# Kernel optimization log

Measured on AMD Instinct MI355X. Metric: run time of the kernel, lower is better.

The kernel has to match this reference:

```python
import jax, jax.numpy as jnp
import numpy as np

LN_EPS = 1e-5
TOP_K = 2

def _layer_norm(x, g, b):
    m = jnp.mean(x, axis=-1, keepdims=True)
    v = jnp.var(x, axis=-1, keepdims=True)
    return (x - m) * jax.lax.rsqrt(v + LN_EPS) * g + b

def _skew(X, pad_value):
    # shift every row one step right: [B,M,L] -> [B,M,M+L]
    B, M, L = X.shape
    X = jnp.pad(X, ((0, 0), (0, 0), (0, M + 1)), constant_values=pad_value)
    X = X.reshape(B, -1)[:, :-M]
    return X.reshape(B, M, M + L)

def _unskew(X):
    # reverse of _skew: [B,M,M+L] -> [B,M,L]
    B, M, Lt = X.shape
    L = Lt - M
    X = X.reshape(B, -1)
    X = jnp.pad(X, ((0, 0), (0, M)))
    return X.reshape(B, M, M + L + 1)[:, :, :L]

def _heads(x, K, D):
    # [B,T,H] -> [B*K,T,D]
    B, T, _ = x.shape
    return x.reshape(B, T, K, D).transpose(0, 2, 1, 3).reshape(B * K, T, D)

def setup_inputs() -> dict:
    key = jax.random.key(0)
    ks = jax.random.split(key, 12)
    B, M, L, H, Dh, E, Kh = 4, 512, 512, 1024, 2048, 8, 8
    D = H // Kh
    s = 0.02
    return {
        "h": jax.random.normal(ks[0], (B, M, H), jnp.float32),
        "h_cache": jax.random.normal(ks[1], (B, L, H), jnp.float32),
        "key_pe": jax.random.normal(ks[2], (1, D, L), jnp.float32) * s,
        "Wq": jax.random.normal(ks[3], (H, H), jnp.float32) * s,
        "Wk": jax.random.normal(ks[4], (H, H), jnp.float32) * s,
        "Wv": jax.random.normal(ks[5], (H, H), jnp.float32) * s,
        "Wo": jax.random.normal(ks[6], (H, H), jnp.float32) * s,
        "ln1_g": jnp.ones((H,), jnp.float32),
        "ln1_b": jnp.zeros((H,), jnp.float32),
        "gate_W": jax.random.normal(ks[7], (H, E), jnp.float32) * s,
        "gate_b": jnp.zeros((E,), jnp.float32),
        "W1": jax.random.normal(ks[8], (E, H, Dh), jnp.float32) * s,
        "b1": jnp.zeros((E, Dh), jnp.float32),
        "W2": jax.random.normal(ks[9], (E, Dh, H), jnp.float32) * s,
        "b2": jnp.zeros((E, H), jnp.float32),
        "ln2_g": jnp.ones((H,), jnp.float32),
        "ln2_b": jnp.zeros((H,), jnp.float32),
    }

def reference(h, h_cache, key_pe, Wq, Wk, Wv, Wo, ln1_g, ln1_b,
              gate_W, gate_b, W1, b1, W2, b2, ln2_g, ln2_b):
    B, M, H = h.shape
    L = h_cache.shape[1]
    Kh = 8
    D = H // Kh
    # --- multi-head relative-position attention over (cache, current) ---
    h_all = jnp.concatenate([h_cache, h], axis=1)            # [B, L+M, H]
    q = _heads(h @ Wq, Kh, D)                                # [B*K, M, D]
    k = _heads(h_all @ Wk, Kh, D)                            # [B*K, M+L, D]
    v = _heads(h_all @ Wv, Kh, D)                            # [B*K, M+L, D]
    attn_cont = _unskew(jnp.einsum('bmd,bnd->bmn', q, k))    # [B*K, M, L]
    attn_pos = jnp.einsum('bmd,xdl->bml', q, key_pe)         # [B*K, M, L]
    attn = jax.nn.softmax((attn_cont + attn_pos) / jnp.sqrt(jnp.float32(D)), axis=-1)
    out = jnp.einsum('bmn,bnd->bmd', _skew(attn, 0.0), v)    # [B*K, M, D]
    out = out.reshape(B, Kh, M, D).transpose(0, 2, 1, 3).reshape(B, M, H)
    attn_out = out @ Wo
    h1 = _layer_norm(h + attn_out, ln1_g, ln1_b)             # post-LN residual
    # --- top-k gated MoE FFN (NaiveGate), post-LN residual ---
    x = h1.reshape(-1, H)                                    # [N, H]
    N = x.shape[0]
    E = gate_b.shape[0]
    logits = x @ gate_W + gate_b                             # [N, E]
    top_val, top_idx = jax.lax.top_k(logits, TOP_K)          # [N, k]
    scores = jax.nn.softmax(top_val, axis=-1)                # [N, k]
    combine = jnp.zeros((N, E), x.dtype).at[jnp.arange(N)[:, None], top_idx].add(scores)
    he = jax.nn.relu(jnp.einsum('nh,ehf->enf', x, W1) + b1[:, None, :])  # [E, N, Dh]
    ye = jnp.einsum('enf,efh->enh', he, W2) + b2[:, None, :]             # [E, N, H]
    core = jnp.einsum('ne,enh->nh', combine, ye).reshape(B, M, H)
    output = _layer_norm(h1 + core, ln2_g, ln2_b)
    return output, top_idx
```

## Files before the change

kernel.cpp:

```cpp
#include <hip/hip_runtime.h>
#include <hip/hip_bf16.h>
#include <stdint.h>


typedef _Float16 f16;
typedef _Float16 f16x8 __attribute__((ext_vector_type(8)));
typedef _Float16 f16x4 __attribute__((ext_vector_type(4)));
typedef float    f32x4 __attribute__((ext_vector_type(4)));
typedef int      i32x4 __attribute__((ext_vector_type(4)));

#define MFMA16(a, b, c) __builtin_amdgcn_mfma_f32_16x16x32_f16((a), (b), (c), 0, 0, 0)
#define LO_SCALE 2048.0f
#define LO_INV   4.8828125e-4f

__device__ __forceinline__ void split2(float x, f16* h, f16* l) {
  f16 hh = (f16)x;
  *h = hh;
  *l = (f16)((x - (float)hh) * LO_SCALE);
}

__device__ __forceinline__ f32x4 zero4() {
  f32x4 z; z[0] = 0.f; z[1] = 0.f; z[2] = 0.f; z[3] = 0.f; return z;
}

__global__ void __launch_bounds__(256) cast_hall_k(const float* __restrict__ h,
                                                   const float* __restrict__ hc,
                                                   f16* __restrict__ hi,
                                                   f16* __restrict__ lo) {
  int c = blockIdx.x * 256 + threadIdx.x;
  int e0 = c * 8;
  int row = e0 >> 10;
  int col = e0 & 1023;
  int b = row >> 10, pos = row & 1023;
  const float* src = (pos < 512) ? (hc + (size_t)((b << 9) + pos) * 1024 + col)
                                 : (h  + (size_t)((b << 9) + (pos - 512)) * 1024 + col);
  float4 v0 = ((const float4*)src)[0];
  float4 v1 = ((const float4*)src)[1];
  float xs[8] = {v0.x, v0.y, v0.z, v0.w, v1.x, v1.y, v1.z, v1.w};
  f16x8 vh, vl;
#pragma unroll
  for (int i = 0; i < 8; i++) { f16 a, bb; split2(xs[i], &a, &bb); vh[i] = a; vl[i] = bb; }
  *(f16x8*)&hi[e0] = vh;
  *(f16x8*)&lo[e0] = vl;
}

template <int SPLIT>
__global__ void __launch_bounds__(256) transpose_cast_k(const float* __restrict__ in,
                                                        f16* __restrict__ oh,
                                                        f16* __restrict__ ol,
                                                        int R, int C) {
  in += (size_t)blockIdx.z * R * C;
  oh += (size_t)blockIdx.z * R * C;
  if constexpr (SPLIT) ol += (size_t)blockIdx.z * R * C;
  __shared__ float tile[32][33];
  int c0 = blockIdx.x * 32, r0 = blockIdx.y * 32;
  int tr = threadIdx.x >> 3, tc = (threadIdx.x & 7) * 4;
  float4 v = *(const float4*)&in[(size_t)(r0 + tr) * C + c0 + tc];
  tile[tr][tc + 0] = v.x; tile[tr][tc + 1] = v.y; tile[tr][tc + 2] = v.z; tile[tr][tc + 3] = v.w;
  __syncthreads();
  int oc = tr;
  int orr = tc;
  f16x4 vh, vl;
#pragma unroll
  for (int i = 0; i < 4; i++) {
    float x = tile[orr + i][oc];
    f16 a, bb; split2(x, &a, &bb);
    vh[i] = a; vl[i] = bb;
  }
  *(f16x4*)&oh[(size_t)(c0 + oc) * R + r0 + orr] = vh;
  if constexpr (SPLIT) *(f16x4*)&ol[(size_t)(c0 + oc) * R + r0 + orr] = vl;
}

#define AM_ID 0
#define AM_Q  1
#define AM_GA 2
#define AM_PA 3
#define EP_QK 0
#define EP_VT 1
#define EP_F32 2
#define EP_HE 3
#define EP_YE 4

template <int SPLIT, int AMAP, int EPI>
__global__ void __launch_bounds__(256) gemm_k(
    const f16* __restrict__ Ah, const f16* __restrict__ Al,
    const f16* __restrict__ Bh, const f16* __restrict__ Bl,
    void* __restrict__ o0, void* __restrict__ o1,
    const float* __restrict__ bias,
    int Kd, int strideA, int lgRPB, int bExpStride,
    const int* __restrict__ list, const int* __restrict__ bases,
    const int* __restrict__ counts) {
  constexpr int PL = SPLIT ? 2 : 1;
  constexpr int BN = SPLIT ? 64 : 128;
  constexpr int NT = BN / 32;
  const int e = blockIdx.z;
  int cnt = 0, base0 = 0;
  if constexpr (AMAP == AM_GA || AMAP == AM_PA) {
    cnt = counts[e]; base0 = bases[e];
    if ((int)blockIdx.y * 128 >= cnt) return;
    Bh += (size_t)e * bExpStride;
  }
  __shared__ f16 sA[PL][128 * 32];
  __shared__ f16 sB[PL][BN * 32];
  const int n0 = blockIdx.x * BN, r0 = blockIdx.y * 128;
  const int tid = threadIdx.x, lane = tid & 63, wv = tid >> 6;
  const int wm = (wv >> 1) * 64, wn = (wv & 1) * (BN / 2);

  f32x4 accM[4][NT], accC[4][NT];
#pragma unroll
  for (int i = 0; i < 4; i++)
#pragma unroll
    for (int j = 0; j < NT; j++) { accM[i][j] = zero4(); accC[i][j] = zero4(); }

  int aRow[2], aCu[2];
#pragma unroll
  for (int c = 0; c < 2; c++) {
    int u = c * 256 + tid;
    int r = u >> 2, cu = u & 3;
    aCu[c] = ((cu ^ ((r >> 1) & 3)) << 3);
    int rr = r0 + r;
    int g;
    if constexpr (AMAP == AM_ID) g = rr;
    else if constexpr (AMAP == AM_Q) g = ((rr >> 9) << 10) + 512 + (rr & 511);
    else if constexpr (AMAP == AM_GA) g = (rr < cnt) ? list[base0 + rr] : 0;
    else g = base0 + rr;
    aRow[c] = g;
  }

  for (int k0 = 0; k0 < Kd; k0 += 32) {
#pragma unroll
    for (int c = 0; c < 2; c++) {
      int u = c * 256 + tid;
      int scol = k0 + aCu[c];
      *(f16x8*)&sA[0][u * 8] = *(const f16x8*)&Ah[(size_t)aRow[c] * strideA + scol];
      if constexpr (SPLIT)
        *(f16x8*)&sA[1][u * 8] = *(const f16x8*)&Al[(size_t)aRow[c] * strideA + scol];
    }
#pragma unroll
    for (int c = 0; c * 256 < BN * 4; c++) {
      int u = c * 256 + tid;
      int r = u >> 2, cu = u & 3;
      int scol = k0 + ((cu ^ ((r >> 1) & 3)) << 3);
      int gb = n0 + r;
      *(f16x8*)&sB[0][u * 8] = *(const f16x8*)&Bh[(size_t)gb * Kd + scol];
      if constexpr (SPLIT)
        *(f16x8*)&sB[1][u * 8] = *(const f16x8*)&Bl[(size_t)gb * Kd + scol];
    }
    __syncthreads();

    f16x8 ah[4], al[4];
#pragma unroll
    for (int mt = 0; mt < 4; mt++) {
      int r = wm + mt * 16 + (lane & 15);
      int cu = (lane >> 4) ^ ((r >> 1) & 3);
      ah[mt] = *(const f16x8*)&sA[0][(r * 4 + cu) * 8];
      if constexpr (SPLIT) al[mt] = *(const f16x8*)&sA[1][(r * 4 + cu) * 8];
    }
#pragma unroll
    for (int nt = 0; nt < NT; nt++) {
      int r = wn + nt * 16 + (lane & 15);
      int cu = (lane >> 4) ^ ((r >> 1) & 3);
      f16x8 bh = *(const f16x8*)&sB[0][(r * 4 + cu) * 8];
      f16x8 bl;
      if constexpr (SPLIT) bl = *(const f16x8*)&sB[1][(r * 4 + cu) * 8];
#pragma unroll
      for (int mt = 0; mt < 4; mt++) {
        accM[mt][nt] = MFMA16(ah[mt], bh, accM[mt][nt]);
        if constexpr (SPLIT) {
          accC[mt][nt] = MFMA16(ah[mt], bl, accC[mt][nt]);
          accC[mt][nt] = MFMA16(al[mt], bh, accC[mt][nt]);
        }
      }
    }
    __syncthreads();
  }

#pragma unroll
  for (int mt = 0; mt < 4; mt++)
#pragma unroll
    for (int nt = 0; nt < NT; nt++)
#pragma unroll
      for (int rg = 0; rg < 4; rg++) {
        int row = r0 + wm + mt * 16 + ((lane >> 4) << 2) + rg;
        int col = n0 + wn + nt * 16 + (lane & 15);
        float v = accM[mt][nt][rg];
        if constexpr (SPLIT) v += accC[mt][nt][rg] * LO_INV;
        if constexpr (EPI == EP_QK) {
          int bq = row >> lgRPB, pos = row & ((1 << lgRPB) - 1);
          size_t ad = ((size_t)((((bq << 3) + (col >> 7)) << lgRPB) + pos)) * 128 + (col & 127);
          f16 hh, ll; split2(v, &hh, &ll);
          ((f16*)o0)[ad] = hh; ((f16*)o1)[ad] = ll;
        } else if constexpr (EPI == EP_VT) {
          size_t ad = ((size_t)(((row >> 10) << 3) + (col >> 7)) * 128 + (col & 127)) * 1024 + (row & 1023);
          f16 hh, ll; split2(v, &hh, &ll);
          ((f16*)o0)[ad] = hh; ((f16*)o1)[ad] = ll;
        } else if constexpr (EPI == EP_F32) {
          ((float*)o0)[(size_t)row * 1024 + col] = v;
        } else if constexpr (EPI == EP_HE) {
          if (row < cnt) {
            float t = v + bias[(e << 11) + col];
            ((f16*)o0)[(size_t)(base0 + row) * 2048 + col] = (f16)fmaxf(t, 0.f);
          }
        } else if constexpr (EPI == EP_YE) {
          if (row < cnt)
            ((float*)o0)[(size_t)(base0 + row) * 1024 + col] = v + bias[(e << 10) + col];
        }
      }
}

__device__ __forceinline__ void unpack_p(const unsigned* sp, f16x8* hi, f16x8* lo) {
  i32x4 u0 = *(const i32x4*)sp;
  i32x4 u1 = *(const i32x4*)(sp + 4);
  i32x4 h, l;
  h[0] = (u0[0] & 0xffff) | (u0[1] << 16);
  h[1] = (u0[2] & 0xffff) | (u0[3] << 16);
  h[2] = (u1[0] & 0xffff) | (u1[1] << 16);
  h[3] = (u1[2] & 0xffff) | (u1[3] << 16);
  l[0] = (int)(((unsigned)u0[0] >> 16) | ((unsigned)u0[1] & 0xffff0000u));
  l[1] = (int)(((unsigned)u0[2] >> 16) | ((unsigned)u0[3] & 0xffff0000u));
  l[2] = (int)(((unsigned)u1[0] >> 16) | ((unsigned)u1[1] & 0xffff0000u));
  l[3] = (int)(((unsigned)u1[2] >> 16) | ((unsigned)u1[3] & 0xffff0000u));
  *hi = __builtin_bit_cast(f16x8, h);
  *lo = __builtin_bit_cast(f16x8, l);
}

__global__ void __launch_bounds__(256) attn_k(
    const f16* __restrict__ qh_, const f16* __restrict__ ql_,
    const f16* __restrict__ kh_, const f16* __restrict__ kl_,
    const f16* __restrict__ ph_, const f16* __restrict__ pl_,
    const f16* __restrict__ vh_, const f16* __restrict__ vl_,
    f16* __restrict__ oh_, f16* __restrict__ ol_) {
  __shared__ float S[32][548];
  const int bh = blockIdx.y;
  const int m0 = blockIdx.x * 32;
  const int tid = threadIdx.x, lane = tid & 63, wv = tid >> 6;
  const int lr = lane & 15, lgp = lane >> 4;

  f16x8 qh[2][4], ql[2][4];
  {
    const size_t qbase = ((size_t)bh * 512 + m0) * 128;
#pragma unroll
    for (int mt = 0; mt < 2; mt++)
#pragma unroll
      for (int kb = 0; kb < 4; kb++) {
        size_t off = qbase + (size_t)(mt * 16 + lr) * 128 + kb * 32 + lgp * 8;
        qh[mt][kb] = *(const f16x8*)&qh_[off];
        ql[mt][kb] = *(const f16x8*)&ql_[off];
      }
  }

  {
    const size_t kbase = ((size_t)bh * 1024 + m0) * 128;
    int ntB = (wv < 2) ? wv * 9 : 18 + (wv - 2) * 8;
    int ntE = ntB + ((wv < 2) ? 9 : 8);
    for (int nt = ntB; nt < ntE; ++nt) {
      f16x8 kh[4], kl[4];
#pragma unroll
      for (int kb = 0; kb < 4; kb++) {
        size_t off = kbase + (size_t)(nt * 16 + lr) * 128 + kb * 32 + lgp * 8;
        kh[kb] = *(const f16x8*)&kh_[off];
        kl[kb] = *(const f16x8*)&kl_[off];
      }
      f32x4 aM[2], aC[2];
      aM[0] = zero4(); aM[1] = zero4(); aC[0] = zero4(); aC[1] = zero4();
#pragma unroll
      for (int kb = 0; kb < 4; kb++)
#pragma unroll
        for (int mt = 0; mt < 2; mt++) {
          aM[mt] = MFMA16(qh[mt][kb], kh[kb], aM[mt]);
          aC[mt] = MFMA16(qh[mt][kb], kl[kb], aC[mt]);
          aC[mt] = MFMA16(ql[mt][kb], kh[kb], aC[mt]);
        }
#pragma unroll
      for (int mt = 0; mt < 2; mt++)
#pragma unroll
        for (int rg = 0; rg < 4; rg++) {
          int m = mt * 16 + lgp * 4 + rg;
          S[m][nt * 16 + lr] = aM[mt][rg] + aC[mt][rg] * LO_INV;
        }
    }
  }
  __syncthreads();

  {
    for (int lt = wv * 8; lt < wv * 8 + 8; ++lt) {
      f16x8 eh[4], el[4];
#pragma unroll
      for (int kb = 0; kb < 4; kb++) {
        size_t off = (size_t)(lt * 16 + lr) * 128 + kb * 32 + lgp * 8;
        eh[kb] = *(const f16x8*)&ph_[off];
        el[kb] = *(const f16x8*)&pl_[off];
      }
      f32x4 aM[2], aC[2];
      aM[0] = zero4(); aM[1] = zero4(); aC[0] = zero4(); aC[1] = zero4();
#pragma unroll
      for (int kb = 0; kb < 4; kb++)
#pragma unroll
        for (int mt = 0; mt < 2; mt++) {
          aM[mt] = MFMA16(qh[mt][kb], eh[kb], aM[mt]);
          aC[mt] = MFMA16(qh[mt][kb], el[kb], aC[mt]);
          aC[mt] = MFMA16(ql[mt][kb], eh[kb], aC[mt]);
        }
#pragma unroll
      for (int mt = 0; mt < 2; mt++)
#pragma unroll
        for (int rg = 0; rg < 4; rg++) {
          int m = mt * 16 + lgp * 4 + rg;
          int lc = lt * 16 + lr;
          S[m][m + lc] += aM[mt][rg] + aC[mt][rg] * LO_INV;
        }
    }
  }
  __syncthreads();

  {
    const float scl = 0.08838834764831843f;
    for (int rr = 0; rr < 8; ++rr) {
      int m = wv * 8 + rr;
      float mx = -3.0e38f;
#pragma unroll
      for (int it = 0; it < 9; ++it) {
        int j = it * 64 + lane;
        if (j < 544 && j >= m && j < m + 512) mx = fmaxf(mx, S[m][j]);
      }
#pragma unroll
      for (int o = 32; o > 0; o >>= 1) mx = fmaxf(mx, __shfl_xor(mx, o));
      float pv[9]; float sm = 0.f;
#pragma unroll
      for (int it = 0; it < 9; ++it) {
        int j = it * 64 + lane;
        float p = 0.f;
        if (j < 544 && j >= m && j < m + 512) p = expf((S[m][j] - mx) * scl);
        pv[it] = p; sm += p;
      }
#pragma unroll
      for (int o = 32; o > 0; o >>= 1) sm += __shfl_xor(sm, o);
      float inv = 1.0f / sm;
#pragma unroll
      for (int it = 0; it < 9; ++it) {
        int j = it * 64 + lane;
        if (j < 544) {
          float pn = pv[it] * inv;
          f16 hh, ll; split2(pn, &hh, &ll);
          unsigned pk = (unsigned)__builtin_bit_cast(unsigned short, hh) |
                        ((unsigned)__builtin_bit_cast(unsigned short, ll) << 16);
          ((unsigned*)&S[m][0])[j] = pk;
        }
      }
    }
  }
  __syncthreads();

  f32x4 accM[2][2], accC[2][2];
#pragma unroll
  for (int i = 0; i < 2; i++)
#pragma unroll
    for (int j = 0; j < 2; j++) { accM[i][j] = zero4(); accC[i][j] = zero4(); }
  for (int kb = 0; kb < 17; ++kb) {
    f16x8 pah[2], pal[2];
#pragma unroll
    for (int mt = 0; mt < 2; mt++) {
      const unsigned* sp = (const unsigned*)&S[mt * 16 + lr][0] + kb * 32 + lgp * 8;
      unpack_p(sp, &pah[mt], &pal[mt]);
    }
#pragma unroll
    for (int ntl = 0; ntl < 2; ++ntl) {
      int d = wv * 32 + ntl * 16 + lr;
      size_t off = ((size_t)bh * 128 + d) * 1024 + m0 + kb * 32 + lgp * 8;
      f16x8 vh = *(const f16x8*)&vh_[off];
      f16x8 vl = *(const f16x8*)&vl_[off];
#pragma unroll
      for (int mt = 0; mt < 2; mt++) {
        accM[mt][ntl] = MFMA16(pah[mt], vh, accM[mt][ntl]);
        accC[mt][ntl] = MFMA16(pah[mt], vl, accC[mt][ntl]);
        accC[mt][ntl] = MFMA16(pal[mt], vh, accC[mt][ntl]);
      }
    }
  }
  const int b = bh >> 3, hd = bh & 7;
#pragma unroll
  for (int mt = 0; mt < 2; mt++)
#pragma unroll
    for (int ntl = 0; ntl < 2; ntl++)
#pragma unroll
      for (int rg = 0; rg < 4; rg++) {
        int m = mt * 16 + lgp * 4 + rg;
        int d = wv * 32 + ntl * 16 + lr;
        float v = accM[mt][ntl][rg] + accC[mt][ntl][rg] * LO_INV;
        size_t ad = ((size_t)(b * 512 + m0 + m)) * 1024 + hd * 128 + d;
        f16 hh, ll; split2(v, &hh, &ll);
        oh_[ad] = hh; ol_[ad] = ll;
      }
}

__device__ __forceinline__ float blk_sum(float v, float* red) {
#pragma unroll
  for (int o = 32; o > 0; o >>= 1) v += __shfl_xor(v, o);
  int wv = threadIdx.x >> 6;
  if ((threadIdx.x & 63) == 0) red[wv] = v;
  __syncthreads();
  float r = red[0] + red[1] + red[2] + red[3];
  __syncthreads();
  return r;
}

__global__ void __launch_bounds__(256) ln1_k(const float* __restrict__ h,
                                             const float* __restrict__ ap,
                                             const float* __restrict__ g,
                                             const float* __restrict__ bb,
                                             float* __restrict__ h1,
                                             f16* __restrict__ h1h) {
  int row = blockIdx.x;
  __shared__ float red[4];
  float4 hv = ((const float4*)(h + (size_t)row * 1024))[threadIdx.x];
  float4 av = ((const float4*)(ap + (size_t)row * 1024))[threadIdx.x];
  float4 x; x.x = hv.x + av.x; x.y = hv.y + av.y; x.z = hv.z + av.z; x.w = hv.w + av.w;
  float s = x.x + x.y + x.z + x.w;
  s = blk_sum(s, red);
  float mean = s * (1.0f / 1024.0f);
  float4 d; d.x = x.x - mean; d.y = x.y - mean; d.z = x.z - mean; d.w = x.w - mean;
  float s2 = d.x * d.x + d.y * d.y + d.z * d.z + d.w * d.w;
  s2 = blk_sum(s2, red);
  float var = s2 * (1.0f / 1024.0f);
  float inv = 1.0f / sqrtf(var + 1e-5f);
  float4 gv = ((const float4*)g)[threadIdx.x];
  float4 bv = ((const float4*)bb)[threadIdx.x];
  float4 y; y.x = d.x * inv * gv.x + bv.x; y.y = d.y * inv * gv.y + bv.y;
  y.z = d.z * inv * gv.z + bv.z; y.w = d.w * inv * gv.w + bv.w;
  ((float4*)(h1 + (size_t)row * 1024))[threadIdx.x] = y;
  f16x4 yh; yh[0] = (f16)y.x; yh[1] = (f16)y.y; yh[2] = (f16)y.z; yh[3] = (f16)y.w;
  *(f16x4*)&h1h[(size_t)row * 1024 + threadIdx.x * 4] = yh;
}

__global__ void __launch_bounds__(256) gate_k(const float* __restrict__ h1,
                                              const float* __restrict__ gW,
                                              const float* __restrict__ gb,
                                              float* __restrict__ outIdx,
                                              float* __restrict__ sc,
                                              int* __restrict__ te,
                                              int* __restrict__ ctrl) {
  int t = blockIdx.x * 4 + (threadIdx.x >> 6);
  int lane = threadIdx.x & 63;
  float a0 = 0, a1 = 0, a2 = 0, a3 = 0, a4 = 0, a5 = 0, a6 = 0, a7 = 0;
  for (int i = lane; i < 1024; i += 64) {
    float x = h1[(size_t)t * 1024 + i];
    const float4* w = (const float4*)&gW[i * 8];
    float4 w0 = w[0], w1 = w[1];
    a0 += x * w0.x; a1 += x * w0.y; a2 += x * w0.z; a3 += x * w0.w;
    a4 += x * w1.x; a5 += x * w1.y; a6 += x * w1.z; a7 += x * w1.w;
  }
  float av[8] = {a0, a1, a2, a3, a4, a5, a6, a7};
#pragma unroll
  for (int e = 0; e < 8; e++)
#pragma unroll
    for (int o = 32; o > 0; o >>= 1) av[e] += __shfl_xor(av[e], o);
  if (lane == 0) {
#pragma unroll
    for (int e = 0; e < 8; e++) av[e] += gb[e];
    int i0 = 0; float v0 = av[0];
#pragma unroll
    for (int e = 1; e < 8; e++) if (av[e] > v0) { v0 = av[e]; i0 = e; }
    int i1 = -1; float v1 = -3.0e38f;
#pragma unroll
    for (int e = 0; e < 8; e++) if (e != i0 && av[e] > v1) { v1 = av[e]; i1 = e; }
    float ex = expf(v1 - v0);
    float den = 1.0f + ex;
    outIdx[t * 2] = (float)i0; outIdx[t * 2 + 1] = (float)i1;
    sc[t * 2] = 1.0f / den; sc[t * 2 + 1] = ex / den;
    te[t * 2] = i0; te[t * 2 + 1] = i1;
    atomicAdd(&ctrl[i0], 1); atomicAdd(&ctrl[i1], 1);
  }
}

__global__ void scan_k(int* ctrl) {
  if (threadIdx.x == 0 && blockIdx.x == 0) {
    int s = 0;
    for (int e = 0; e < 8; e++) { ctrl[8 + e] = s; s += ctrl[e]; }
  }
}

__global__ void __launch_bounds__(256) scatter_k(const int* __restrict__ te,
                                                 int* ctrl,
                                                 int* __restrict__ list,
                                                 int* __restrict__ ppos) {
  int t = blockIdx.x * 256 + threadIdx.x;
  if (t >= 2048) return;
#pragma unroll
  for (int s = 0; s < 2; s++) {
    int e = te[t * 2 + s];
    int pos = atomicAdd(&ctrl[16 + e], 1);
    int pr = ctrl[8 + e] + pos;
    list[pr] = t;
    ppos[t * 2 + s] = pr;
  }
}

__global__ void __launch_bounds__(256) comb_ln2_k(const float* __restrict__ h1,
                                                  const float* __restrict__ ye,
                                                  const float* __restrict__ sc,
                                                  const int* __restrict__ ppos,
                                                  const float* __restrict__ g,
                                                  const float* __restrict__ bb,
                                                  float* __restrict__ out) {
  int row = blockIdx.x;
  __shared__ float red[4];
  int p0 = ppos[row * 2], p1 = ppos[row * 2 + 1];
  float s0 = sc[row * 2], s1 = sc[row * 2 + 1];
  float4 a = ((const float4*)(h1 + (size_t)row * 1024))[threadIdx.x];
  float4 y0 = ((const float4*)(ye + (size_t)p0 * 1024))[threadIdx.x];
  float4 y1 = ((const float4*)(ye + (size_t)p1 * 1024))[threadIdx.x];
  float4 x;
  x.x = a.x + s0 * y0.x + s1 * y1.x; x.y = a.y + s0 * y0.y + s1 * y1.y;
  x.z = a.z + s0 * y0.z + s1 * y1.z; x.w = a.w + s0 * y0.w + s1 * y1.w;
  float s = x.x + x.y + x.z + x.w;
  s = blk_sum(s, red);
  float mean = s * (1.0f / 1024.0f);
  float4 d; d.x = x.x - mean; d.y = x.y - mean; d.z = x.z - mean; d.w = x.w - mean;
  float s2 = d.x * d.x + d.y * d.y + d.z * d.z + d.w * d.w;
  s2 = blk_sum(s2, red);
  float var = s2 * (1.0f / 1024.0f);
  float inv = 1.0f / sqrtf(var + 1e-5f);
  float4 gv = ((const float4*)g)[threadIdx.x];
  float4 bv = ((const float4*)bb)[threadIdx.x];
  float4 y; y.x = d.x * inv * gv.x + bv.x; y.y = d.y * inv * gv.y + bv.y;
  y.z = d.z * inv * gv.z + bv.z; y.w = d.w * inv * gv.w + bv.w;
  ((float4*)(out + (size_t)row * 1024))[threadIdx.x] = y;
}

extern "C" void kernel_launch(void* const* d_in, const int* in_sizes, int n_in,
                              void* d_out, int out_size, void* d_ws, size_t ws_size,
                              hipStream_t stream) {
  const float* h   = (const float*)d_in[0];
  const float* hc  = (const float*)d_in[1];
  const float* pe  = (const float*)d_in[2];
  const float* Wq  = (const float*)d_in[3];
  const float* Wk  = (const float*)d_in[4];
  const float* Wv  = (const float*)d_in[5];
  const float* Wo  = (const float*)d_in[6];
  const float* g1  = (const float*)d_in[7];
  const float* b1n = (const float*)d_in[8];
  const float* gW  = (const float*)d_in[9];
  const float* gb  = (const float*)d_in[10];
  const float* W1  = (const float*)d_in[11];
  const float* b1e = (const float*)d_in[12];
  const float* W2  = (const float*)d_in[13];
  const float* b2e = (const float*)d_in[14];
  const float* g2  = (const float*)d_in[15];
  const float* b2n = (const float*)d_in[16];
  float* out = (float*)d_out;
  float* outIdx = out + 2097152;

  char* w = (char*)d_ws;
  size_t off = 0;
  auto alloc = [&](size_t bytes) -> char* {
    char* p = w + off;
    off += (bytes + 255) & ~(size_t)255;
    return p;
  };
  int*   ctrl  = (int*)alloc(128);
  f16*   hallH = (f16*)alloc(4096ull * 1024 * 2);
  f16*   hallL = (f16*)alloc(4096ull * 1024 * 2);
  f16*   WqtH  = (f16*)alloc(1024ull * 1024 * 2);
  f16*   WqtL  = (f16*)alloc(1024ull * 1024 * 2);
  f16*   WktH  = (f16*)alloc(1024ull * 1024 * 2);
  f16*   WktL  = (f16*)alloc(1024ull * 1024 * 2);
  f16*   WvtH  = (f16*)alloc(1024ull * 1024 * 2);
  f16*   WvtL  = (f16*)alloc(1024ull * 1024 * 2);
  f16*   WotH  = (f16*)alloc(1024ull * 1024 * 2);
  f16*   WotL  = (f16*)alloc(1024ull * 1024 * 2);
  f16*   peH   = (f16*)alloc(512ull * 128 * 2);
  f16*   peL   = (f16*)alloc(512ull * 128 * 2);
  f16*   qH    = (f16*)alloc(2097152ull * 2);
  f16*   qL    = (f16*)alloc(2097152ull * 2);
  f16*   kH    = (f16*)alloc(4194304ull * 2);
  f16*   kL    = (f16*)alloc(4194304ull * 2);
  f16*   vtH   = (f16*)alloc(4194304ull * 2);
  f16*   vtL   = (f16*)alloc(4194304ull * 2);
  f16*   attH  = (f16*)alloc(2097152ull * 2);
  f16*   attL  = (f16*)alloc(2097152ull * 2);
  float* aproj = (float*)alloc(2097152ull * 4);
  float* h1    = (float*)alloc(2097152ull * 4);
  f16*   h1h   = (f16*)alloc(2097152ull * 2);
  f16*   W1t   = (f16*)alloc(16777216ull * 2);
  f16*   W2t   = (f16*)alloc(16777216ull * 2);
  f16*   he    = (f16*)alloc(4224ull * 2048 * 2);
  float* ye    = (float*)alloc(4224ull * 1024 * 4);
  float* scb   = (float*)alloc(2048ull * 2 * 4);
  int*   te    = (int*)alloc(2048ull * 2 * 4);
  int*   ppos  = (int*)alloc(2048ull * 2 * 4);
  int*   list  = (int*)alloc(4096ull * 4);
  (void)in_sizes; (void)n_in; (void)out_size; (void)ws_size;

  hipMemsetAsync(ctrl, 0, 128, stream);

  cast_hall_k<<<2048, 256, 0, stream>>>(h, hc, hallH, hallL);
  transpose_cast_k<1><<<dim3(32, 32, 1), 256, 0, stream>>>(Wq, WqtH, WqtL, 1024, 1024);
  transpose_cast_k<1><<<dim3(32, 32, 1), 256, 0, stream>>>(Wk, WktH, WktL, 1024, 1024);
  transpose_cast_k<1><<<dim3(32, 32, 1), 256, 0, stream>>>(Wv, WvtH, WvtL, 1024, 1024);
  transpose_cast_k<1><<<dim3(32, 32, 1), 256, 0, stream>>>(Wo, WotH, WotL, 1024, 1024);
  transpose_cast_k<1><<<dim3(16, 4, 1), 256, 0, stream>>>(pe, peH, peL, 128, 512);
  transpose_cast_k<0><<<dim3(64, 32, 8), 256, 0, stream>>>(W1, W1t, nullptr, 1024, 2048);
  transpose_cast_k<0><<<dim3(32, 64, 8), 256, 0, stream>>>(W2, W2t, nullptr, 2048, 1024);

  gemm_k<1, AM_Q, EP_QK><<<dim3(16, 16, 1), 256, 0, stream>>>(
      hallH, hallL, WqtH, WqtL, qH, qL, nullptr, 1024, 1024, 9, 0, nullptr, nullptr, nullptr);
  gemm_k<1, AM_ID, EP_QK><<<dim3(16, 32, 1), 256, 0, stream>>>(
      hallH, hallL, WktH, WktL, kH, kL, nullptr, 1024, 1024, 10, 0, nullptr, nullptr, nullptr);
  gemm_k<1, AM_ID, EP_VT><<<dim3(16, 32, 1), 256, 0, stream>>>(
      hallH, hallL, WvtH, WvtL, vtH, vtL, nullptr, 1024, 1024, 10, 0, nullptr, nullptr, nullptr);

  attn_k<<<dim3(16, 32, 1), 256, 0, stream>>>(qH, qL, kH, kL, peH, peL, vtH, vtL, attH, attL);

  gemm_k<1, AM_ID, EP_F32><<<dim3(16, 16, 1), 256, 0, stream>>>(
      attH, attL, WotH, WotL, aproj, nullptr, nullptr, 1024, 1024, 0, 0, nullptr, nullptr, nullptr);
  ln1_k<<<2048, 256, 0, stream>>>(h, aproj, g1, b1n, h1, h1h);

  gate_k<<<512, 256, 0, stream>>>(h1, gW, gb, outIdx, scb, te, ctrl);
  scan_k<<<1, 64, 0, stream>>>(ctrl);
  scatter_k<<<8, 256, 0, stream>>>(te, ctrl, list, ppos);

  gemm_k<0, AM_GA, EP_HE><<<dim3(16, 16, 8), 256, 0, stream>>>(
      h1h, nullptr, W1t, nullptr, he, nullptr, b1e, 1024, 1024, 0, 2048 * 1024, list, ctrl + 8, ctrl);
  gemm_k<0, AM_PA, EP_YE><<<dim3(8, 16, 8), 256, 0, stream>>>(
      he, nullptr, W2t, nullptr, ye, nullptr, b2e, 2048, 2048, 0, 1024 * 2048, nullptr, ctrl + 8, ctrl);

  comb_ln2_k<<<2048, 256, 0, stream>>>(h1, ye, scb, ppos, g2, b2n, out);
}
```

Baseline: 646.0 us.

## Fuse Q/K/V projections into one GEMM and retile the other GEMMs

Concatenates the transposed Wq/Wk/Wv into a single 3072-wide weight so one GEMM launch computes Q, K and V over all 4096 rows. The epilogue routes each column segment to its Q, K or transposed-V layout, and drops Q rows that come from the cache. The GEMM template now takes BM/BN tile sizes, and the output projection and both MoE GEMMs use 64-row tiles to launch more blocks. This cuts launch count and raises occupancy, at the cost of computing Q for the 2048 cache rows that are then discarded.

```diff
diff --git a/kernel.cpp b/kernel.cpp
--- a/kernel.cpp
+++ b/kernel.cpp
@@ -72,56 +72,55 @@
 }
 
 #define AM_ID 0
-#define AM_Q  1
 #define AM_GA 2
 #define AM_PA 3
-#define EP_QK 0
-#define EP_VT 1
+#define EP_QKV 0
 #define EP_F32 2
 #define EP_HE 3
 #define EP_YE 4
 
-template <int SPLIT, int AMAP, int EPI>
+template <int SPLIT, int BM, int BN, int AMAP, int EPI>
 __global__ void __launch_bounds__(256) gemm_k(
     const f16* __restrict__ Ah, const f16* __restrict__ Al,
     const f16* __restrict__ Bh, const f16* __restrict__ Bl,
     void* __restrict__ o0, void* __restrict__ o1,
     const float* __restrict__ bias,
-    int Kd, int strideA, int lgRPB, int bExpStride,
+    int Kd, int strideA, int bExpStride,
     const int* __restrict__ list, const int* __restrict__ bases,
     const int* __restrict__ counts) {
   constexpr int PL = SPLIT ? 2 : 1;
-  constexpr int BN = SPLIT ? 64 : 128;
+  constexpr int MT = BM / 32;
   constexpr int NT = BN / 32;
+  constexpr int AIT = BM / 64;
+  constexpr int BIT = BN / 64;
   const int e = blockIdx.z;
   int cnt = 0, base0 = 0;
   if constexpr (AMAP == AM_GA || AMAP == AM_PA) {
     cnt = counts[e]; base0 = bases[e];
-    if ((int)blockIdx.y * 128 >= cnt) return;
+    if ((int)blockIdx.y * BM >= cnt) return;
     Bh += (size_t)e * bExpStride;
   }
-  __shared__ f16 sA[PL][128 * 32];
+  __shared__ f16 sA[PL][BM * 32];
   __shared__ f16 sB[PL][BN * 32];
-  const int n0 = blockIdx.x * BN, r0 = blockIdx.y * 128;
+  const int n0 = blockIdx.x * BN, r0 = blockIdx.y * BM;
   const int tid = threadIdx.x, lane = tid & 63, wv = tid >> 6;
-  const int wm = (wv >> 1) * 64, wn = (wv & 1) * (BN / 2);
-
-  f32x4 accM[4][NT], accC[4][NT];
-#pragma unroll
-  for (int i = 0; i < 4; i++)
+  const int wm = (wv >> 1) * (BM / 2), wn = (wv & 1) * (BN / 2);
+
+  f32x4 accM[MT][NT], accC[MT][NT];
+#pragma unroll
+  for (int i = 0; i < MT; i++)
 #pragma unroll
     for (int j = 0; j < NT; j++) { accM[i][j] = zero4(); accC[i][j] = zero4(); }
 
-  int aRow[2], aCu[2];
-#pragma unroll
-  for (int c = 0; c < 2; c++) {
+  int aRow[AIT], aCu[AIT];
+#pragma unroll
+  for (int c = 0; c < AIT; c++) {
     int u = c * 256 + tid;
     int r = u >> 2, cu = u & 3;
     aCu[c] = ((cu ^ ((r >> 1) & 3)) << 3);
     int rr = r0 + r;
     int g;
     if constexpr (AMAP == AM_ID) g = rr;
-    else if constexpr (AMAP == AM_Q) g = ((rr >> 9) << 10) + 512 + (rr & 511);
     else if constexpr (AMAP == AM_GA) g = (rr < cnt) ? list[base0 + rr] : 0;
     else g = base0 + rr;
     aRow[c] = g;
@@ -129,7 +128,7 @@
 
   for (int k0 = 0; k0 < Kd; k0 += 32) {
 #pragma unroll
-    for (int c = 0; c < 2; c++) {
+    for (int c = 0; c < AIT; c++) {
       int u = c * 256 + tid;
       int scol = k0 + aCu[c];
       *(f16x8*)&sA[0][u * 8] = *(const f16x8*)&Ah[(size_t)aRow[c] * strideA + scol];
@@ -137,7 +136,7 @@
         *(f16x8*)&sA[1][u * 8] = *(const f16x8*)&Al[(size_t)aRow[c] * strideA + scol];
     }
 #pragma unroll
-    for (int c = 0; c * 256 < BN * 4; c++) {
+    for (int c = 0; c < BIT; c++) {
       int u = c * 256 + tid;
       int r = u >> 2, cu = u & 3;
       int scol = k0 + ((cu ^ ((r >> 1) & 3)) << 3);
@@ -148,9 +147,9 @@
     }
     __syncthreads();
 
-    f16x8 ah[4], al[4];
-#pragma unroll
-    for (int mt = 0; mt < 4; mt++) {
+    f16x8 ah[MT], al[MT];
+#pragma unroll
+    for (int mt = 0; mt < MT; mt++) {
       int r = wm + mt * 16 + (lane & 15);
       int cu = (lane >> 4) ^ ((r >> 1) & 3);
       ah[mt] = *(const f16x8*)&sA[0][(r * 4 + cu) * 8];
@@ -164,7 +163,7 @@
       f16x8 bl;
       if constexpr (SPLIT) bl = *(const f16x8*)&sB[1][(r * 4 + cu) * 8];
 #pragma unroll
-      for (int mt = 0; mt < 4; mt++) {
+      for (int mt = 0; mt < MT; mt++) {
         accM[mt][nt] = MFMA16(ah[mt], bh, accM[mt][nt]);
         if constexpr (SPLIT) {
           accC[mt][nt] = MFMA16(ah[mt], bl, accC[mt][nt]);
@@ -176,7 +175,7 @@
   }
 
 #pragma unroll
-  for (int mt = 0; mt < 4; mt++)
+  for (int mt = 0; mt < MT; mt++)
 #pragma unroll
     for (int nt = 0; nt < NT; nt++)
 #pragma unroll
@@ -185,15 +184,28 @@
         int col = n0 + wn + nt * 16 + (lane & 15);
         float v = accM[mt][nt][rg];
         if constexpr (SPLIT) v += accC[mt][nt][rg] * LO_INV;
-        if constexpr (EPI == EP_QK) {
-          int bq = row >> lgRPB, pos = row & ((1 << lgRPB) - 1);
-          size_t ad = ((size_t)((((bq << 3) + (col >> 7)) << lgRPB) + pos)) * 128 + (col & 127);
+        if constexpr (EPI == EP_QKV) {
+          f16* QH = (f16*)o0;
+          f16* QL = QH + (1u << 21);
+          f16* KH = QL + (1u << 21);
+          f16* KL = KH + (1u << 22);
+          f16* VTH = KL + (1u << 22);
+          f16* VTL = VTH + (1u << 22);
+          int b = row >> 10, pos = row & 1023;
+          int seg = col >> 10, hd = (col >> 7) & 7, d = col & 127;
           f16 hh, ll; split2(v, &hh, &ll);
-          ((f16*)o0)[ad] = hh; ((f16*)o1)[ad] = ll;
-        } else if constexpr (EPI == EP_VT) {
-          size_t ad = ((size_t)(((row >> 10) << 3) + (col >> 7)) * 128 + (col & 127)) * 1024 + (row & 1023);
-          f16 hh, ll; split2(v, &hh, &ll);
-          ((f16*)o0)[ad] = hh; ((f16*)o1)[ad] = ll;
+          if (seg == 0) {
+            if (pos >= 512) {
+              size_t ad = ((size_t)((((b << 3) + hd) << 9) + (pos - 512))) * 128 + d;
+              QH[ad] = hh; QL[ad] = ll;
+            }
+          } else if (seg == 1) {
+            size_t ad = ((size_t)((((b << 3) + hd) << 10) + pos)) * 128 + d;
+            KH[ad] = hh; KL[ad] = ll;
+          } else {
+            size_t ad = ((size_t)((((b << 3) + hd) << 7) + d)) * 1024 + pos;
+            VTH[ad] = hh; VTL[ad] = ll;
+          }
         } else if constexpr (EPI == EP_F32) {
           ((float*)o0)[(size_t)row * 1024 + col] = v;
         } else if constexpr (EPI == EP_HE) {
@@ -557,25 +569,22 @@
     off += (bytes + 255) & ~(size_t)255;
     return p;
   };
-  int*   ctrl  = (int*)alloc(128);
-  f16*   hallH = (f16*)alloc(4096ull * 1024 * 2);
-  f16*   hallL = (f16*)alloc(4096ull * 1024 * 2);
-  f16*   WqtH  = (f16*)alloc(1024ull * 1024 * 2);
-  f16*   WqtL  = (f16*)alloc(1024ull * 1024 * 2);
-  f16*   WktH  = (f16*)alloc(1024ull * 1024 * 2);
-  f16*   WktL  = (f16*)alloc(1024ull * 1024 * 2);
-  f16*   WvtH  = (f16*)alloc(1024ull * 1024 * 2);
-  f16*   WvtL  = (f16*)alloc(1024ull * 1024 * 2);
-  f16*   WotH  = (f16*)alloc(1024ull * 1024 * 2);
-  f16*   WotL  = (f16*)alloc(1024ull * 1024 * 2);
-  f16*   peH   = (f16*)alloc(512ull * 128 * 2);
-  f16*   peL   = (f16*)alloc(512ull * 128 * 2);
-  f16*   qH    = (f16*)alloc(2097152ull * 2);
-  f16*   qL    = (f16*)alloc(2097152ull * 2);
-  f16*   kH    = (f16*)alloc(4194304ull * 2);
-  f16*   kL    = (f16*)alloc(4194304ull * 2);
-  f16*   vtH   = (f16*)alloc(4194304ull * 2);
-  f16*   vtL   = (f16*)alloc(4194304ull * 2);
+  int*   ctrl    = (int*)alloc(128);
+  f16*   hallH   = (f16*)alloc(4096ull * 1024 * 2);
+  f16*   hallL   = (f16*)alloc(4096ull * 1024 * 2);
+  f16*   WqkvtH  = (f16*)alloc(3072ull * 1024 * 2);
+  f16*   WqkvtL  = (f16*)alloc(3072ull * 1024 * 2);
+  f16*   WotH    = (f16*)alloc(1024ull * 1024 * 2);
+  f16*   WotL    = (f16*)alloc(1024ull * 1024 * 2);
+  f16*   peH     = (f16*)alloc(512ull * 128 * 2);
+  f16*   peL     = (f16*)alloc(512ull * 128 * 2);
+  f16*   qkv     = (f16*)alloc(20971520ull * 2);
+  f16*   qH  = qkv;
+  f16*   qL  = qH + (1u << 21);
+  f16*   kH  = qL + (1u << 21);
+  f16*   kL  = kH + (1u << 22);
+  f16*   vtH = kL + (1u << 22);
+  f16*   vtL = vtH + (1u << 22);
   f16*   attH  = (f16*)alloc(2097152ull * 2);
   f16*   attL  = (f16*)alloc(2097152ull * 2);
   float* aproj = (float*)alloc(2097152ull * 4);
@@ -594,35 +603,35 @@
   hipMemsetAsync(ctrl, 0, 128, stream);
 
   cast_hall_k<<<2048, 256, 0, stream>>>(h, hc, hallH, hallL);
-  transpose_cast_k<1><<<dim3(32, 32, 1), 256, 0, stream>>>(Wq, WqtH, WqtL, 1024, 1024);
-  transpose_cast_k<1><<<dim3(32, 32, 1), 256, 0, stream>>>(Wk, WktH, WktL, 1024, 1024);
-  transpose_cast_k<1><<<dim3(32, 32, 1), 256, 0, stream>>>(Wv, WvtH, WvtL, 1024, 1024);
+  transpose_cast_k<1><<<dim3(32, 32, 1), 256, 0, stream>>>(Wq, WqkvtH, WqkvtL, 1024, 1024);
+  transpose_cast_k<1><<<dim3(32, 32, 1), 256, 0, stream>>>(Wk, WqkvtH + 1048576, WqkvtL + 1048576, 1024, 1024);
+  transpose_cast_k<1><<<dim3(32, 32, 1), 256, 0, stream>>>(Wv, WqkvtH + 2097152, WqkvtL + 2097152, 1024, 1024);
   transpose_cast_k<1><<<dim3(32, 32, 1), 256, 0, stream>>>(Wo, WotH, WotL, 1024, 1024);
   transpose_cast_k<1><<<dim3(16, 4, 1), 256, 0, stream>>>(pe, peH, peL, 128, 512);
   transpose_cast_k<0><<<dim3(64, 32, 8), 256, 0, stream>>>(W1, W1t, nullptr, 1024, 2048);
   transpose_cast_k<0><<<dim3(32, 64, 8), 256, 0, stream>>>(W2, W2t, nullptr, 2048, 1024);
 
-  gemm_k<1, AM_Q, EP_QK><<<dim3(16, 16, 1), 256, 0, stream>>>(
-      hallH, hallL, WqtH, WqtL, qH, qL, nullptr, 1024, 1024, 9, 0, nullptr, nullptr, nullptr);
-  gemm_k<1, AM_ID, EP_QK><<<dim3(16, 32, 1), 256, 0, stream>>>(
-      hallH, hallL, WktH, WktL, kH, kL, nullptr, 1024, 1024, 10, 0, nullptr, nullptr, nullptr);
-  gemm_k<1, AM_ID, EP_VT><<<dim3(16, 32, 1), 256, 0, stream>>>(
-      hallH, hallL, WvtH, WvtL, vtH, vtL, nullptr, 1024, 1024, 10, 0, nullptr, nullptr, nullptr);
+  gemm_k<1, 128, 64, AM_ID, EP_QKV><<<dim3(48, 32, 1), 256, 0, stream>>>(
+      hallH, hallL, WqkvtH, WqkvtL, qkv, nullptr, nullptr, 1024, 1024, 0,
+      nullptr, nullptr, nullptr);
 
   attn_k<<<dim3(16, 32, 1), 256, 0, stream>>>(qH, qL, kH, kL, peH, peL, vtH, vtL, attH, attL);
 
-  gemm_k<1, AM_ID, EP_F32><<<dim3(16, 16, 1), 256, 0, stream>>>(
-      attH, attL, WotH, WotL, aproj, nullptr, nullptr, 1024, 1024, 0, 0, nullptr, nullptr, nullptr);
+  gemm_k<1, 64, 64, AM_ID, EP_F32><<<dim3(16, 32, 1), 256, 0, stream>>>(
+      attH, attL, WotH, WotL, aproj, nullptr, nullptr, 1024, 1024, 0,
+      nullptr, nullptr, nullptr);
   ln1_k<<<2048, 256, 0, stream>>>(h, aproj, g1, b1n, h1, h1h);
 
   gate_k<<<512, 256, 0, stream>>>(h1, gW, gb, outIdx, scb, te, ctrl);
   scan_k<<<1, 64, 0, stream>>>(ctrl);
   scatter_k<<<8, 256, 0, stream>>>(te, ctrl, list, ppos);
 
-  gemm_k<0, AM_GA, EP_HE><<<dim3(16, 16, 8), 256, 0, stream>>>(
-      h1h, nullptr, W1t, nullptr, he, nullptr, b1e, 1024, 1024, 0, 2048 * 1024, list, ctrl + 8, ctrl);
-  gemm_k<0, AM_PA, EP_YE><<<dim3(8, 16, 8), 256, 0, stream>>>(
-      he, nullptr, W2t, nullptr, ye, nullptr, b2e, 2048, 2048, 0, 1024 * 2048, nullptr, ctrl + 8, ctrl);
+  gemm_k<0, 64, 128, AM_GA, EP_HE><<<dim3(16, 32, 8), 256, 0, stream>>>(
+      h1h, nullptr, W1t, nullptr, he, nullptr, b1e, 1024, 1024, 2048 * 1024,
+      list, ctrl + 8, ctrl);
+  gemm_k<0, 64, 128, AM_PA, EP_YE><<<dim3(8, 32, 8), 256, 0, stream>>>(
+      he, nullptr, W2t, nullptr, ye, nullptr, b2e, 2048, 2048, 1024 * 2048,
+      nullptr, ctrl + 8, ctrl);
 
   comb_ln2_k<<<2048, 256, 0, stream>>>(h1, ye, scb, ppos, g2, b2n, out);
 }
```

New measurement: 666.1 us. 1.03x slower.
